# Kernel tuning notes

Measured on AMD Instinct MI355X. Metric: run time of the kernel, lower is better.

The kernel has to match this reference:

```python
import jax, jax.numpy as jnp
import numpy as np

B, INPUT_LEN, F_IN = 32, 4096, 256
N = B * INPUT_LEN          # 131072 total nodes in the flattened batch
E = 4_194_304              # ~avg degree 32
HID, OUT = 3, 1            # GCNConv(256->3) then GCNConv(3->1), per source code
PRED_LEN = 1024


def setup_inputs() -> dict:
    key = jax.random.key(0)
    k = jax.random.split(key, 5)
    node_features = jax.random.normal(k[0], (B, INPUT_LEN, F_IN), dtype=jnp.float32)
    # flattened, already-offset edge index (Batch.from_data_list result)
    edge_index = jax.random.randint(k[1], (2, E), 0, N, dtype=jnp.int32)
    W1 = jax.random.normal(k[2], (F_IN, HID), dtype=jnp.float32) / np.float32(np.sqrt(F_IN))
    b1 = jnp.zeros((HID,), dtype=jnp.float32)
    W2 = jax.random.normal(k[3], (HID, OUT), dtype=jnp.float32) / np.float32(np.sqrt(HID))
    b2 = jnp.zeros((OUT,), dtype=jnp.float32)
    return {"node_features": node_features, "W1": W1, "b1": b1, "W2": W2, "b2": b2,
            "edge_index": edge_index, "pred_len": PRED_LEN, "input_len": INPUT_LEN}


def _gcn_norm(edge_index, num_nodes, dtype):
    # PyG gcn_norm: add self-loops, deg over destination, symmetric deg^-1/2 norm
    loop = jnp.arange(num_nodes, dtype=edge_index.dtype)
    src = jnp.concatenate([edge_index[0], loop])
    dst = jnp.concatenate([edge_index[1], loop])
    deg = jax.ops.segment_sum(jnp.ones_like(src, dtype=dtype), dst, num_segments=num_nodes)
    dinv = jnp.where(deg > 0, jax.lax.rsqrt(deg), 0.0).astype(dtype)
    norm = dinv[src] * dinv[dst]  # [E+N]
    return src, dst, norm


def _gcn_conv(x, src, dst, norm, W, b, num_nodes):
    h = x @ W                              # [N, out] linear first (small out dim)
    msg = h[src] * norm[:, None]           # gather + scale per edge
    out = jax.ops.segment_sum(msg, dst, num_segments=num_nodes)  # scatter-add
    return out + b


def reference(node_features, W1, b1, W2, b2, edge_index, pred_len, input_len):
    n_nodes = node_features.shape[0] * node_features.shape[1]
    x = node_features.reshape(n_nodes, node_features.shape[2])
    src, dst, norm = _gcn_norm(edge_index, n_nodes, x.dtype)
    h = jax.nn.relu(_gcn_conv(x, src, dst, norm, W1, b1, n_nodes))
    h = _gcn_conv(h, src, dst, norm, W2, b2, n_nodes)
    h = h.reshape(-1, input_len, h.shape[1])   # [B, input_len, num_target]
    return h[:, :pred_len, :]
```

## Files before the change

### kernel.cpp

```cpp
#include <hip/hip_runtime.h>
#include <hip/hip_bf16.h>
#include <stdint.h>

#define F_IN 256
#define QSCALE 512.0f
#define QBIAS  8192
#define FMASK  0x1FFFFFull
#define H2Q    16384.0f
#define NBUK   16
#define BCAP   524288
#define LCAP   128
#define BUCKB  4096
#define DEGSTG_OFF (32u << 20)
#define STG1_OFF   (34u << 20)
#define STG2_OFF   (50u << 20)
#define SCRATCH_SZ (52u << 20)

typedef short short8 __attribute__((ext_vector_type(8)));
typedef float floatx4 __attribute__((ext_vector_type(4)));

__device__ __forceinline__ float bf2f(unsigned short u) {
    union { unsigned int i; float f; } v; v.i = ((unsigned int)u) << 16; return v.f;
}
__device__ __forceinline__ unsigned short f2bf(float f) {
    union { unsigned int i; float f; } v; v.f = f;
    unsigned int r = v.i + 0x7FFF + ((v.i >> 16) & 1);
    return (unsigned short)(r >> 16);
}
__device__ __forceinline__ unsigned long long packq(float v0, float v1, float v2) {
    int m0 = __float2int_rn(v0 * QSCALE);
    int m1 = __float2int_rn(v1 * QSCALE);
    int m2 = __float2int_rn(v2 * QSCALE);
    m0 = max(-4095, min(4095, m0));
    m1 = max(-4095, min(4095, m1));
    m2 = max(-4095, min(4095, m2));
    return (unsigned long long)(unsigned)(m0 + QBIAS)
         | ((unsigned long long)(unsigned)(m1 + QBIAS) << 21)
         | ((unsigned long long)(unsigned)(m2 + QBIAS) << 42);
}

__global__ void k_init(unsigned int* __restrict__ gcur,
                       const unsigned int* __restrict__ w1w,
                       const unsigned short* __restrict__ w1us,
                       unsigned short* __restrict__ w1t,
                       int* __restrict__ flag) {
    __shared__ int cnt;
    if (threadIdx.x == 0) cnt = 0;
    if (threadIdx.x < NBUK) gcur[threadIdx.x] = 0u;
    __syncthreads();
    int local = 0;
    for (int i = threadIdx.x; i < 384; i += blockDim.x) {
        unsigned e = (w1w[i] >> 7) & 0xFF;
        if (e >= 100 && e <= 135) local++;
    }
    atomicAdd(&cnt, local);
    __syncthreads();
    if (threadIdx.x == 0) *flag = (2 * cnt < 384) ? 1 : 0;
    int k = threadIdx.x;
    #pragma unroll
    for (int n = 0; n < 16; n++)
        w1t[n * 256 + k] = (n < 3) ? w1us[k * 3 + n] : 0;
}

__global__ void __launch_bounds__(256)
k_bucket_gemv(int buckB, int gemvB,
              const int* __restrict__ src, const int* __restrict__ dst,
              unsigned int* __restrict__ xbuf, unsigned int* __restrict__ gcur,
              const void* __restrict__ xv_, const void* __restrict__ w1_,
              const unsigned short* __restrict__ w1t,
              unsigned short* __restrict__ h1con,
              const int* __restrict__ flag, int N) {
    __shared__ unsigned int lbuf[NBUK][LCAP];
    __shared__ unsigned int lcnt[NBUK];
    __shared__ unsigned int lbase[NBUK];
    int b = blockIdx.x;
    if (b < buckB) {
        if (threadIdx.x < NBUK) lcnt[threadIdx.x] = 0u;
        __syncthreads();
        int g4 = b * 256 + threadIdx.x;
        int4 s4 = ((const int4*)src)[g4];
        int4 d4 = ((const int4*)dst)[g4];
        #pragma unroll
        for (int u = 0; u < 4; u++) {
            int s = (u == 0) ? s4.x : (u == 1) ? s4.y : (u == 2) ? s4.z : s4.w;
            int d = (u == 0) ? d4.x : (u == 1) ? d4.y : (u == 2) ? d4.z : d4.w;
            unsigned p = ((unsigned)s << 13) | ((unsigned)d & 8191u);
            int bk = ((unsigned)d) >> 13;
            unsigned lp = atomicAdd(&lcnt[bk], 1u);
            if (lp < LCAP) lbuf[bk][lp] = p;
            else {
                unsigned g = atomicAdd(&gcur[bk], 1u);
                xbuf[(size_t)bk * BCAP + g] = p;
            }
        }
        __syncthreads();
        if (threadIdx.x < NBUK) {
            unsigned c = min(lcnt[threadIdx.x], (unsigned)LCAP);
            lcnt[threadIdx.x] = c;
            lbase[threadIdx.x] = atomicAdd(&gcur[threadIdx.x], c);
        }
        __syncthreads();
        for (int bk = 0; bk < NBUK; bk++) {
            unsigned c = lcnt[bk], base = lbase[bk];
            for (unsigned i = threadIdx.x; i < c; i += 256)
                xbuf[(size_t)bk * BCAP + base + i] = lbuf[bk][i];
        }
        return;
    }
    int wave = threadIdx.x >> 6;
    int lane = threadIdx.x & 63;
    int row0 = (b - buckB) * 64 + wave * 16;
    if (row0 >= N) return;
    int f32mode = *flag;
    int m = lane & 15, quad = lane >> 4;

    if (!f32mode) {
        const short* xs = (const short*)xv_;
        const short* ap = xs + (size_t)(row0 + m) * F_IN + quad * 8;
        const short* bp = (const short*)w1t + m * 256 + quad * 8;
        floatx4 acc = {0.f, 0.f, 0.f, 0.f};
        #pragma unroll
        for (int s = 0; s < 8; s++) {
            short8 av = *(const short8*)(ap + s * 32);
            short8 bv = *(const short8*)(bp + s * 32);
            acc = __builtin_amdgcn_mfma_f32_16x16x32_bf16(av, bv, acc, 0, 0, 0);
        }
        if (m < 3) {
            #pragma unroll
            for (int r = 0; r < 4; r++)
                h1con[4 * (size_t)(row0 + quad * 4 + r) + m] = f2bf(acc[r]);
        }
    } else {
        const float* xf = (const float*)xv_;
        const float4* wr = (const float4*)w1_;
        float4 wa = wr[lane*3+0], wb = wr[lane*3+1], wc = wr[lane*3+2];
        float w00 = wa.x, w01 = wa.y, w02 = wa.z, w10 = wa.w;
        float w11 = wb.x, w12 = wb.y, w20 = wb.z, w21 = wb.w;
        float w22 = wc.x, w30 = wc.y, w31 = wc.z, w32 = wc.w;
        for (int r = 0; r < 16; r++) {
            int row = row0 + r;
            float4 xv = ((const float4*)(xf + (size_t)row * F_IN))[lane];
            float p0 = xv.x*w00 + xv.y*w10 + xv.z*w20 + xv.w*w30;
            float p1 = xv.x*w01 + xv.y*w11 + xv.z*w21 + xv.w*w31;
            float p2 = xv.x*w02 + xv.y*w12 + xv.z*w22 + xv.w*w32;
            #pragma unroll
            for (int off = 32; off; off >>= 1) {
                p0 += __shfl_down(p0, off, 64);
                p1 += __shfl_down(p1, off, 64);
                p2 += __shfl_down(p2, off, 64);
            }
            if (lane == 0) {
                ushort4 o;
                o.x = f2bf(p0); o.y = f2bf(p1); o.z = f2bf(p2); o.w = 0;
                ((ushort4*)h1con)[row] = o;
            }
        }
    }
}

__global__ void __launch_bounds__(256)
k_bhist(const unsigned int* __restrict__ xbuf, const unsigned int* __restrict__ gcur,
        unsigned int* __restrict__ degstg) {
    __shared__ unsigned int cnt8[2048];
    int bucket = blockIdx.x & 15, sub = blockIdx.x >> 4;
    for (int i = threadIdx.x; i < 2048; i += 256) cnt8[i] = 0u;
    __syncthreads();
    unsigned cnt = gcur[bucket];
    unsigned e0 = (unsigned)(((unsigned long long)sub       * cnt) >> 4);
    unsigned e1 = (unsigned)(((unsigned long long)(sub + 1) * cnt) >> 4);
    const unsigned int* bp = xbuf + (size_t)bucket * BCAP;
    for (unsigned i = e0 + threadIdx.x; i < e1; i += 256) {
        unsigned q = bp[i] & 8191u;
        atomicAdd(&cnt8[q >> 2], 1u << ((q & 3u) << 3));
    }
    __syncthreads();
    unsigned int* out = degstg + (size_t)blockIdx.x * 2048;
    for (int i = threadIdx.x; i < 2048; i += 256) out[i] = cnt8[i];
}

__global__ void k_dinvpack(const unsigned char* __restrict__ degstg,
                           unsigned char* __restrict__ deg8, float* __restrict__ dinv,
                           unsigned long long* __restrict__ h1con, int N) {
    int n = blockIdx.x * blockDim.x + threadIdx.x;
    if (n >= N) return;
    int bk = n >> 13, idx = n & 8191;
    unsigned deg = 1u;
    #pragma unroll
    for (int s = 0; s < 16; s++)
        deg += degstg[(size_t)((s << 4) | bk) * 8192 + idx];
    deg8[n] = (unsigned char)deg;
    float dv = rsqrtf((float)deg);
    dinv[n] = dv;
    ushort4 h = ((const ushort4*)h1con)[n];
    h1con[n] = packq(bf2f(h.x) * dv, bf2f(h.y) * dv, bf2f(h.z) * dv);
}

__global__ void __launch_bounds__(1024)
k_scatter1(const unsigned int* __restrict__ xbuf,
           const unsigned long long* __restrict__ con,
           unsigned long long* __restrict__ stg1,
           const unsigned int* __restrict__ gcur) {
    __shared__ unsigned long long acc[8192];
    int bucket = blockIdx.x & 15, sub = blockIdx.x >> 4;
    for (int i = threadIdx.x; i < 8192; i += 1024) acc[i] = 0ull;
    __syncthreads();
    unsigned cnt = gcur[bucket];
    unsigned e0 = (unsigned)(((unsigned long long)sub       * cnt) >> 4);
    unsigned e1 = (unsigned)(((unsigned long long)(sub + 1) * cnt) >> 4);
    const unsigned int* bp = xbuf + (size_t)bucket * BCAP;
    for (unsigned i = e0 + threadIdx.x; i < e1; i += 1024) {
        unsigned p = bp[i];
        atomicAdd(&acc[p & 8191u], con[p >> 13]);
    }
    __syncthreads();
    unsigned long long* out = stg1 + (size_t)blockIdx.x * 8192;
    for (int i = threadIdx.x; i < 8192; i += 1024) out[i] = acc[i];
}

__global__ void k_rlin2(const unsigned long long* __restrict__ stg1,
                        const unsigned long long* __restrict__ con,
                        const unsigned char* __restrict__ deg8,
                        const float* __restrict__ dinv,
                        const void* __restrict__ b1_, const void* __restrict__ w2_,
                        int* __restrict__ h2q, const int* __restrict__ flag, int N) {
    int n = blockIdx.x * blockDim.x + threadIdx.x;
    if (n >= N) return;
    int f32mode = *flag;
    float b10, b11, b12, w20, w21, w22;
    if (f32mode) {
        const float* b1 = (const float*)b1_; const float* w2 = (const float*)w2_;
        b10 = b1[0]; b11 = b1[1]; b12 = b1[2];
        w20 = w2[0]; w21 = w2[1]; w22 = w2[2];
    } else {
        const unsigned short* b1 = (const unsigned short*)b1_;
        const unsigned short* w2 = (const unsigned short*)w2_;
        b10 = bf2f(b1[0]); b11 = bf2f(b1[1]); b12 = bf2f(b1[2]);
        w20 = bf2f(w2[0]); w21 = bf2f(w2[1]); w22 = bf2f(w2[2]);
    }
    int bk = n >> 13, idx = n & 8191;
    unsigned long long T = con[n];
    #pragma unroll
    for (int s = 0; s < 16; s++)
        T += stg1[(size_t)((s << 4) | bk) * 8192 + idx];
    long long dbias = (long long)deg8[n] * QBIAS;
    float q = 1.0f / QSCALE;
    float s0 = (float)((long long)( T        & FMASK) - dbias) * q;
    float s1 = (float)((long long)((T >> 21) & FMASK) - dbias) * q;
    float s2 = (float)((long long)((T >> 42) & FMASK) - dbias) * q;
    float dv = dinv[n];
    float a0 = fmaxf(s0 * dv + b10, 0.0f);
    float a1 = fmaxf(s1 * dv + b11, 0.0f);
    float a2 = fmaxf(s2 * dv + b12, 0.0f);
    float h2 = (a0 * w20 + a1 * w21 + a2 * w22) * dv;
    h2q[n] = __float2int_rn(h2 * H2Q);
}

__global__ void __launch_bounds__(1024)
k_scatter2(const unsigned int* __restrict__ xbuf, const int* __restrict__ h2q,
           int* __restrict__ stg2, const unsigned int* __restrict__ gcur) {
    __shared__ int acc[2048];
    int bucket = blockIdx.x & 15, sub = blockIdx.x >> 4;
    for (int i = threadIdx.x; i < 2048; i += 1024) acc[i] = 0;
    __syncthreads();
    unsigned cnt = gcur[bucket];
    unsigned e0 = (unsigned)(((unsigned long long)sub       * cnt) >> 4);
    unsigned e1 = (unsigned)(((unsigned long long)(sub + 1) * cnt) >> 4);
    const unsigned int* bp = xbuf + (size_t)bucket * BCAP;
    for (unsigned i = e0 + threadIdx.x; i < e1; i += 1024) {
        unsigned p = bp[i];
        unsigned low = p & 8191u;
        if ((low & 4095u) < 1024u) {
            int cl = (int)(((low >> 12) << 10) | (low & 1023u));
            atomicAdd(&acc[cl], h2q[p >> 13]);
        }
    }
    __syncthreads();
    int* out = stg2 + (size_t)blockIdx.x * 2048;
    for (int i = threadIdx.x; i < 2048; i += 1024) out[i] = acc[i];
}

__global__ void k_r2out(const int* __restrict__ stg2, const int* __restrict__ h2q,
                        const float* __restrict__ dinv, const void* __restrict__ b2_,
                        void* __restrict__ out_, const int* __restrict__ flag, int M) {
    int t = blockIdx.x * blockDim.x + threadIdx.x;
    if (t >= M) return;
    int f32mode = *flag;
    float b2 = f32mode ? ((const float*)b2_)[0] : bf2f(((const unsigned short*)b2_)[0]);
    int n = ((t >> 10) << 12) | (t & 1023);
    int bk = n >> 13;
    unsigned low = (unsigned)n & 8191u;
    int cl = (int)(((low >> 12) << 10) | (low & 1023u));
    int S = h2q[n];
    #pragma unroll
    for (int s = 0; s < 16; s++)
        S += stg2[(size_t)((s << 4) | bk) * 2048 + cl];
    float v = (float)S * (1.0f / H2Q) * dinv[n] + b2;
    if (f32mode) ((float*)out_)[t] = v;
    else         ((unsigned short*)out_)[t] = f2bf(v);
}

extern "C" void kernel_launch(void* const* d_in, const int* in_sizes, int n_in,
                              void* d_out, int out_size, void* d_ws, size_t ws_size,
                              hipStream_t stream) {
    void*       x   = d_in[0];
    const void* w1  = d_in[1];
    const void* b1  = d_in[2];
    const void* w2  = d_in[3];
    const void* b2  = d_in[4];
    const int* eidx = (const int*)d_in[5];

    const int N = in_sizes[0] / F_IN;
    const int E = in_sizes[5] / 2;
    const int* src = eidx;
    const int* dst = eidx + E;

    char* ws = (char*)d_ws;
    unsigned char*      deg8  = (unsigned char*)(ws);
    float*              dinv  = (float*)(ws + (size_t)N);
    unsigned long long* h1con = (unsigned long long*)(ws + (size_t)5*N);
    int*                h2q   = (int*)(ws + (size_t)13*N);
    int*                flag  = (int*)(ws + (size_t)17*N);
    unsigned int*       gcur  = (unsigned int*)(ws + (size_t)17*N + 128);
    unsigned short*     w1t   = (unsigned short*)(ws + (size_t)17*N + 256);

    bool big_ws = ws_size >= ((size_t)(4u << 20) + SCRATCH_SZ);
    char* scratch = big_ws ? (ws + (4u << 20)) : (char*)x;
    unsigned int*       xbuf   = (unsigned int*)scratch;
    unsigned int*       degstg = (unsigned int*)(scratch + DEGSTG_OFF);
    unsigned long long* stg1   = (unsigned long long*)(scratch + STG1_OFF);
    int*                stg2   = (int*)(scratch + STG2_OFF);

    const int bs = 256;
    int gemvB = N / 64;
    k_init<<<1, bs, 0, stream>>>(gcur, (const unsigned int*)w1,
                                 (const unsigned short*)w1, w1t, flag);
    if (big_ws) {
        k_bucket_gemv<<<BUCKB + gemvB, bs, 0, stream>>>(BUCKB, gemvB, src, dst,
                                                        xbuf, gcur, x, w1, w1t,
                                                        (unsigned short*)h1con, flag, N);
    } else {
        k_bucket_gemv<<<gemvB, bs, 0, stream>>>(0, gemvB, src, dst, xbuf, gcur,
                                                x, w1, w1t,
                                                (unsigned short*)h1con, flag, N);
        k_bucket_gemv<<<BUCKB, bs, 0, stream>>>(BUCKB, 0, src, dst, xbuf, gcur,
                                                x, w1, w1t,
                                                (unsigned short*)h1con, flag, N);
    }
    k_bhist   <<<256, bs, 0, stream>>>(xbuf, gcur, degstg);
    k_dinvpack<<<(N + bs-1)/bs, bs, 0, stream>>>((const unsigned char*)degstg,
                                                 deg8, dinv, h1con, N);
    k_scatter1<<<256, 1024, 0, stream>>>(xbuf, h1con, stg1, gcur);
    k_rlin2   <<<(N + bs-1)/bs, bs, 0, stream>>>(stg1, h1con, deg8, dinv, b1, w2,
                                                 h2q, flag, N);
    k_scatter2<<<256, 1024, 0, stream>>>(xbuf, h2q, stg2, gcur);
    k_r2out   <<<(out_size + bs-1)/bs, bs, 0, stream>>>(stg2, h2q, dinv, b2,
                                                        d_out, flag, out_size);
}
```

Measured before the change: 333.1 us.

## Split bucketing from GEMV and fuse GEMV with degree histogram, 1024-thread blocks

Edge bucketing now runs in its own kernel with 1024-thread blocks and a larger shared staging capacity per bucket. The node GEMV is co-launched with the per-bucket degree histogram instead of with bucketing, which removes a separate histogram launch. The aim is fewer global atomics on the bucket cursors, since more edges stay in shared memory, and better overlap of the histogram with the compute-heavy GEMV. The trade-offs are that the bucketing pass can no longer hide behind the GEMV and that larger blocks may lower occupancy.

```diff
diff --git a/kernel.cpp b/kernel.cpp
--- a/kernel.cpp
+++ b/kernel.cpp
@@ -9,8 +9,7 @@
 #define H2Q    16384.0f
 #define NBUK   16
 #define BCAP   524288
-#define LCAP   128
-#define BUCKB  4096
+#define LCAP   384
 #define DEGSTG_OFF (32u << 20)
 #define STG1_OFF   (34u << 20)
 #define STG2_OFF   (50u << 20)
@@ -62,54 +61,74 @@
         w1t[n * 256 + k] = (n < 3) ? w1us[k * 3 + n] : 0;
 }
 
-__global__ void __launch_bounds__(256)
-k_bucket_gemv(int buckB, int gemvB,
-              const int* __restrict__ src, const int* __restrict__ dst,
-              unsigned int* __restrict__ xbuf, unsigned int* __restrict__ gcur,
-              const void* __restrict__ xv_, const void* __restrict__ w1_,
-              const unsigned short* __restrict__ w1t,
-              unsigned short* __restrict__ h1con,
-              const int* __restrict__ flag, int N) {
+__global__ void __launch_bounds__(1024)
+k_bucket(const int* __restrict__ src, const int* __restrict__ dst,
+         unsigned int* __restrict__ xbuf, unsigned int* __restrict__ gcur, int E) {
     __shared__ unsigned int lbuf[NBUK][LCAP];
     __shared__ unsigned int lcnt[NBUK];
     __shared__ unsigned int lbase[NBUK];
+    if (threadIdx.x < NBUK) lcnt[threadIdx.x] = 0u;
+    __syncthreads();
+    int g4 = blockIdx.x * 1024 + threadIdx.x;
+    int4 s4 = ((const int4*)src)[g4];
+    int4 d4 = ((const int4*)dst)[g4];
+    #pragma unroll
+    for (int u = 0; u < 4; u++) {
+        int s = (u == 0) ? s4.x : (u == 1) ? s4.y : (u == 2) ? s4.z : s4.w;
+        int d = (u == 0) ? d4.x : (u == 1) ? d4.y : (u == 2) ? d4.z : d4.w;
+        unsigned p = ((unsigned)s << 13) | ((unsigned)d & 8191u);
+        int bk = ((unsigned)d) >> 13;
+        unsigned lp = atomicAdd(&lcnt[bk], 1u);
+        if (lp < LCAP) lbuf[bk][lp] = p;
+        else {
+            unsigned g = atomicAdd(&gcur[bk], 1u);
+            xbuf[(size_t)bk * BCAP + g] = p;
+        }
+    }
+    __syncthreads();
+    if (threadIdx.x < NBUK) {
+        unsigned c = min(lcnt[threadIdx.x], (unsigned)LCAP);
+        lcnt[threadIdx.x] = c;
+        lbase[threadIdx.x] = atomicAdd(&gcur[threadIdx.x], c);
+    }
+    __syncthreads();
+    for (int bk = 0; bk < NBUK; bk++) {
+        unsigned c = lcnt[bk], base = lbase[bk];
+        for (unsigned i = threadIdx.x; i < c; i += 1024)
+            xbuf[(size_t)bk * BCAP + base + i] = lbuf[bk][i];
+    }
+}
+
+__global__ void __launch_bounds__(1024)
+k_gemv_bhist(int bhistB,
+             const unsigned int* __restrict__ xbuf, const unsigned int* __restrict__ gcur,
+             unsigned int* __restrict__ degstg,
+             const void* __restrict__ xv_, const void* __restrict__ w1_,
+             const unsigned short* __restrict__ w1t,
+             unsigned short* __restrict__ h1con,
+             const int* __restrict__ flag, int N) {
+    __shared__ unsigned int cnt8[2048];
     int b = blockIdx.x;
-    if (b < buckB) {
-        if (threadIdx.x < NBUK) lcnt[threadIdx.x] = 0u;
+    if (b < bhistB) {
+        int bucket = b & 15, sub = b >> 4;
+        for (int i = threadIdx.x; i < 2048; i += 1024) cnt8[i] = 0u;
         __syncthreads();
-        int g4 = b * 256 + threadIdx.x;
-        int4 s4 = ((const int4*)src)[g4];
-        int4 d4 = ((const int4*)dst)[g4];
-        #pragma unroll
-        for (int u = 0; u < 4; u++) {
-            int s = (u == 0) ? s4.x : (u == 1) ? s4.y : (u == 2) ? s4.z : s4.w;
-            int d = (u == 0) ? d4.x : (u == 1) ? d4.y : (u == 2) ? d4.z : d4.w;
-            unsigned p = ((unsigned)s << 13) | ((unsigned)d & 8191u);
-            int bk = ((unsigned)d) >> 13;
-            unsigned lp = atomicAdd(&lcnt[bk], 1u);
-            if (lp < LCAP) lbuf[bk][lp] = p;
-            else {
-                unsigned g = atomicAdd(&gcur[bk], 1u);
-                xbuf[(size_t)bk * BCAP + g] = p;
-            }
+        unsigned cnt = gcur[bucket];
+        unsigned e0 = (unsigned)(((unsigned long long)sub       * cnt) >> 4);
+        unsigned e1 = (unsigned)(((unsigned long long)(sub + 1) * cnt) >> 4);
+        const unsigned int* bp = xbuf + (size_t)bucket * BCAP;
+        for (unsigned i = e0 + threadIdx.x; i < e1; i += 1024) {
+            unsigned q = bp[i] & 8191u;
+            atomicAdd(&cnt8[q >> 2], 1u << ((q & 3u) << 3));
         }
         __syncthreads();
-        if (threadIdx.x < NBUK) {
-            unsigned c = min(lcnt[threadIdx.x], (unsigned)LCAP);
-            lcnt[threadIdx.x] = c;
-            lbase[threadIdx.x] = atomicAdd(&gcur[threadIdx.x], c);
-        }
-        __syncthreads();
-        for (int bk = 0; bk < NBUK; bk++) {
-            unsigned c = lcnt[bk], base = lbase[bk];
-            for (unsigned i = threadIdx.x; i < c; i += 256)
-                xbuf[(size_t)bk * BCAP + base + i] = lbuf[bk][i];
-        }
+        unsigned int* out = degstg + (size_t)b * 2048;
+        for (int i = threadIdx.x; i < 2048; i += 1024) out[i] = cnt8[i];
         return;
     }
     int wave = threadIdx.x >> 6;
     int lane = threadIdx.x & 63;
-    int row0 = (b - buckB) * 64 + wave * 16;
+    int row0 = (b - bhistB) * 256 + wave * 16;
     if (row0 >= N) return;
     int f32mode = *flag;
     int m = lane & 15, quad = lane >> 4;
@@ -158,26 +177,6 @@
     }
 }
 
-__global__ void __launch_bounds__(256)
-k_bhist(const unsigned int* __restrict__ xbuf, const unsigned int* __restrict__ gcur,
-        unsigned int* __restrict__ degstg) {
-    __shared__ unsigned int cnt8[2048];
-    int bucket = blockIdx.x & 15, sub = blockIdx.x >> 4;
-    for (int i = threadIdx.x; i < 2048; i += 256) cnt8[i] = 0u;
-    __syncthreads();
-    unsigned cnt = gcur[bucket];
-    unsigned e0 = (unsigned)(((unsigned long long)sub       * cnt) >> 4);
-    unsigned e1 = (unsigned)(((unsigned long long)(sub + 1) * cnt) >> 4);
-    const unsigned int* bp = xbuf + (size_t)bucket * BCAP;
-    for (unsigned i = e0 + threadIdx.x; i < e1; i += 256) {
-        unsigned q = bp[i] & 8191u;
-        atomicAdd(&cnt8[q >> 2], 1u << ((q & 3u) << 3));
-    }
-    __syncthreads();
-    unsigned int* out = degstg + (size_t)blockIdx.x * 2048;
-    for (int i = threadIdx.x; i < 2048; i += 256) out[i] = cnt8[i];
-}
-
 __global__ void k_dinvpack(const unsigned char* __restrict__ degstg,
                            unsigned char* __restrict__ deg8, float* __restrict__ dinv,
                            unsigned long long* __restrict__ h1con, int N) {
@@ -331,22 +330,24 @@
     int*                stg2   = (int*)(scratch + STG2_OFF);
 
     const int bs = 256;
-    int gemvB = N / 64;
+    int gemvB = N / 256;
     k_init<<<1, bs, 0, stream>>>(gcur, (const unsigned int*)w1,
                                  (const unsigned short*)w1, w1t, flag);
     if (big_ws) {
-        k_bucket_gemv<<<BUCKB + gemvB, bs, 0, stream>>>(BUCKB, gemvB, src, dst,
-                                                        xbuf, gcur, x, w1, w1t,
-                                                        (unsigned short*)h1con, flag, N);
+        k_bucket<<<E / 4096, 1024, 0, stream>>>(src, dst, xbuf, gcur, E);
+        k_gemv_bhist<<<256 + gemvB, 1024, 0, stream>>>(256, xbuf, gcur, degstg,
+                                                       x, w1, w1t,
+                                                       (unsigned short*)h1con,
+                                                       flag, N);
     } else {
-        k_bucket_gemv<<<gemvB, bs, 0, stream>>>(0, gemvB, src, dst, xbuf, gcur,
-                                                x, w1, w1t,
-                                                (unsigned short*)h1con, flag, N);
-        k_bucket_gemv<<<BUCKB, bs, 0, stream>>>(BUCKB, 0, src, dst, xbuf, gcur,
-                                                x, w1, w1t,
-                                                (unsigned short*)h1con, flag, N);
-    }
-    k_bhist   <<<256, bs, 0, stream>>>(xbuf, gcur, degstg);
+        k_gemv_bhist<<<gemvB, 1024, 0, stream>>>(0, nullptr, gcur, degstg,
+                                                 x, w1, w1t,
+                                                 (unsigned short*)h1con, flag, N);
+        k_bucket<<<E / 4096, 1024, 0, stream>>>(src, dst, xbuf, gcur, E);
+        k_gemv_bhist<<<256, 1024, 0, stream>>>(256, xbuf, gcur, degstg,
+                                               x, w1, w1t,
+                                               (unsigned short*)h1con, flag, N);
+    }
     k_dinvpack<<<(N + bs-1)/bs, bs, 0, stream>>>((const unsigned char*)degstg,
                                                  deg8, dinv, h1con, N);
     k_scatter1<<<256, 1024, 0, stream>>>(xbuf, h1con, stg1, gcur);
```

New measurement: 285.9 us. 1.17x faster.
